# Kernel tuning notes

Hardware: AMD Instinct MI355X
Metric: run time of the kernel (lower is better)

## Reference

```python
import jax, jax.numpy as jnp
import numpy as np

B, W, H = 8, 1024, 1024
NUM_LABELS = 100  # mask ids in [0, NUM_LABELS); 0 = background
EPS = 1e-7


def setup_inputs() -> dict:
    key = jax.random.key(0)
    k1, k2 = jax.random.split(key)
    pred = jax.random.normal(k1, (B, 2, W, H), dtype=jnp.float32)
    mask = jax.random.randint(k2, (B, W, H), 0, NUM_LABELS, dtype=jnp.int32)
    ignored_map = jnp.ones((B, W, H), dtype=jnp.float32)
    return {"pred": pred, "mask": mask, "ignored_map": ignored_map}


def _smooth_l1(d):
    # SmoothL1Loss(reduction='none'), beta=1
    a = jnp.abs(d)
    return jnp.where(a < 1.0, 0.5 * d * d, a - 0.5)


def _gt_single(mask2d):
    # Vectorized replacement of the per-instance python loop:
    # segment-mean for centroids, segment-max for the per-instance `norm`.
    seg = mask2d.reshape(-1)  # [W*H]
    x_map = jnp.tile(jnp.arange(H, dtype=jnp.float32), W)    # column index (x)
    y_map = jnp.repeat(jnp.arange(W, dtype=jnp.float32), H)  # row index (y)
    cnt = jax.ops.segment_sum(jnp.ones_like(x_map), seg, num_segments=NUM_LABELS)
    safe_cnt = jnp.maximum(cnt, 1.0)
    xc = (jax.ops.segment_sum(x_map, seg, num_segments=NUM_LABELS) / safe_cnt)[seg]
    yc = (jax.ops.segment_sum(y_map, seg, num_segments=NUM_LABELS) / safe_cnt)[seg]
    fg = (seg != 0).astype(jnp.float32)  # label 0 is background (index_list[1:])
    vx = (x_map - xc) * fg  # (x_map - mean_x) * nuclei, instances are disjoint
    vy = (y_map - yc) * fg
    # torch.max over the whole image of (coord - c)*nuclei == max(seg_max, 0)
    mx = jnp.maximum(jax.ops.segment_max(vx, seg, num_segments=NUM_LABELS), 0.0)
    my = jnp.maximum(jax.ops.segment_max(vy, seg, num_segments=NUM_LABELS), 0.0)
    gx = vx / jnp.where(mx == 0.0, 1.0, mx)[seg]  # norm(): divide by max iff max != 0
    gy = vy / jnp.where(my == 0.0, 1.0, my)[seg]
    return jnp.stack([gx, gy]).reshape(2, W, H)


def reference(pred, mask, ignored_map):
    gt = jax.vmap(_gt_single)(mask)  # [B, 2, W, H]
    fg = (mask != 0).astype(jnp.float32)[:, None]  # [B, 1, W, H]
    bg = 1.0 - fg
    n = float(mask.size)
    # ((mask != 0) + 1e-07).sum() == fg_count + eps * numel
    fg_den = jnp.sum(fg) + EPS * n
    bg_den = jnp.sum(bg) + EPS * n
    d = _smooth_l1(pred - gt)
    ig = ignored_map[:, None]
    offset_loss = jnp.sum(d * ig * (fg / fg_den + bg / bg_den))
    return offset_loss, gt
```

## Files before the change

kernel.cpp:

```cpp
#include <hip/hip_runtime.h>

#define NL 100
#define BB 8
#define WW 1024
#define HH 1024
#define NPIX (WW * HH)
#define EPSF 1e-7f

#define OFF_CNT 0
#define OFF_SX  800
#define OFF_SY  1600
#define OFF_MX  2400
#define OFF_MY  3200
#define OFF_TAB 4000
#define OFF_INV 7200
#define OFF_M8  7216
#define ZERO_WORDS 4000

template<bool EMIT8>
__global__ __launch_bounds__(256) void k_stats(const int* __restrict__ mask,
                                               int* __restrict__ ws,
                                               unsigned* __restrict__ m8) {
    __shared__ unsigned s_cs[4][NL];
    __shared__ unsigned s_mx[4][NL];
    __shared__ unsigned g_cnt[NL], g_sx[NL], g_sy[NL], g_mx[NL], g_my[NL];
    const int b    = blockIdx.y;
    const int wv   = threadIdx.x >> 6;
    const int lane = threadIdx.x & 63;
    for (int i = threadIdx.x; i < NL; i += 256) {
        g_cnt[i] = 0u; g_sx[i] = 0u; g_sy[i] = 0u; g_mx[i] = 0u; g_my[i] = 0u;
    }
    for (int i = lane; i < NL; i += 64) { s_cs[wv][i] = 0u; s_mx[wv][i] = 0u; }
    __syncthreads();

    const int4* m4  = (const int4*)(mask + (size_t)b * NPIX);
    unsigned*   m8b = m8 + (size_t)b * (NPIX / 4);
    const int y0 = blockIdx.x * 8 + wv * 2;

    int4 R[2][4];
#pragma unroll
    for (int r = 0; r < 2; ++r)
#pragma unroll
        for (int it = 0; it < 4; ++it)
            R[r][it] = m4[(y0 + r) * 256 + it * 64 + lane];

#pragma unroll
    for (int r = 0; r < 2; ++r) {
        const int y = y0 + r;
#pragma unroll
        for (int it = 0; it < 4; ++it) {
            const int4 mv = R[r][it];
            const int c4 = it * 64 + lane;
            const unsigned x0 = (unsigned)(c4 << 2);
            const unsigned v0 = (1u << 21) + x0;
            atomicAdd(&s_cs[wv][mv.x], v0);     atomicMax(&s_mx[wv][mv.x], x0);
            atomicAdd(&s_cs[wv][mv.y], v0 + 1); atomicMax(&s_mx[wv][mv.y], x0 + 1);
            atomicAdd(&s_cs[wv][mv.z], v0 + 2); atomicMax(&s_mx[wv][mv.z], x0 + 2);
            atomicAdd(&s_cs[wv][mv.w], v0 + 3); atomicMax(&s_mx[wv][mv.w], x0 + 3);
            if (EMIT8)
                m8b[y * 256 + c4] = (unsigned)mv.x | ((unsigned)mv.y << 8) |
                                    ((unsigned)mv.z << 16) | ((unsigned)mv.w << 24);
        }
        for (int e = lane; e < NL; e += 64) {
            const unsigned cs  = s_cs[wv][e];
            const unsigned mx  = s_mx[wv][e];
            const unsigned cnt = cs >> 21;
            if (cnt) {
                atomicAdd(&g_cnt[e], cnt);
                atomicAdd(&g_sx[e],  cs & 0x1FFFFFu);
                atomicAdd(&g_sy[e],  cnt * (unsigned)y);
                atomicMax(&g_my[e], (unsigned)y);
            }
            if (mx) atomicMax(&g_mx[e], mx);
            s_cs[wv][e] = 0u;
            s_mx[wv][e] = 0u;
        }
    }
    __syncthreads();
    for (int e = threadIdx.x; e < NL; e += 256) {
        const unsigned cnt = g_cnt[e];
        if (cnt) {
            atomicAdd(&ws[OFF_CNT + b * NL + e], (int)cnt);
            atomicAdd(&ws[OFF_SX  + b * NL + e], (int)g_sx[e]);
            atomicAdd(&ws[OFF_SY  + b * NL + e], (int)g_sy[e]);
            atomicMax(&ws[OFF_MX  + b * NL + e], (int)g_mx[e]);
            atomicMax(&ws[OFF_MY  + b * NL + e], (int)g_my[e]);
        }
    }
}

__global__ void k_final(int* __restrict__ wsi) {
    float* wsf = (float*)wsi;
    const int t = threadIdx.x;
    if (t < BB * NL) {
        const int c = wsi[OFF_CNT + t];
        const float sc = (float)(c > 0 ? c : 1);
        const float xc = (float)wsi[OFF_SX + t] / sc;
        const float yc = (float)wsi[OFF_SY + t] / sc;
        float fmx = (float)wsi[OFF_MX + t] - xc; if (fmx < 0.0f) fmx = 0.0f;
        float fmy = (float)wsi[OFF_MY + t] - yc; if (fmy < 0.0f) fmy = 0.0f;
        float4 e;
        e.x = xc;
        e.y = yc;
        e.z = (fmx == 0.0f) ? 1.0f : 1.0f / fmx;
        e.w = (fmy == 0.0f) ? 1.0f : 1.0f / fmy;
        ((float4*)(wsf + OFF_TAB))[t] = e;
    }
    if (t == 0) {
        long long bg = 0;
        for (int b = 0; b < BB; ++b) bg += wsi[OFF_CNT + b * NL];
        const float n = (float)BB * (float)NPIX;
        const float fg_den = (float)((long long)BB * NPIX - bg) + EPSF * n;
        const float bg_den = (float)bg + EPSF * n;
        wsf[OFF_INV + 0] = 1.0f / fg_den;
        wsf[OFF_INV + 1] = 1.0f / bg_den;
    }
}

template<bool USE8>
__global__ __launch_bounds__(256) void k_loss(const int* __restrict__ mask,
                                              const unsigned* __restrict__ m8,
                                              const float* __restrict__ pred,
                                              const float* __restrict__ ig,
                                              const int* __restrict__ ws,
                                              float* __restrict__ out) {
    const float* wsf = (const float*)ws;
    __shared__ float4 s_tab[NL];
    const int b = blockIdx.y;
    for (int i = threadIdx.x; i < NL; i += 256)
        s_tab[i] = ((const float4*)(wsf + OFF_TAB))[b * NL + i];
    __syncthreads();
    const float inv_fg = wsf[OFF_INV + 0];
    const float inv_bg = wsf[OFF_INV + 1];

    const int4*     mi4 = (const int4*)(mask + (size_t)b * NPIX);
    const unsigned* m8b = m8 + (size_t)b * (NPIX / 4);
    const float4*   ig4 = (const float4*)(ig + (size_t)b * NPIX);
    const float4*   px4 = (const float4*)(pred + (size_t)(2 * b) * NPIX);
    const float4*   py4 = (const float4*)(pred + (size_t)(2 * b + 1) * NPIX);
    float* gx_out = out + 1 + (size_t)(2 * b) * NPIX;
    float* gy_out = out + 1 + (size_t)(2 * b + 1) * NPIX;

    const int base = blockIdx.x * 1024;
    unsigned M8[4]; int4 MI[4]; float4 IV[4], PX[4], PY[4];
#pragma unroll
    for (int it = 0; it < 4; ++it) {
        const int i4 = base + it * 256 + threadIdx.x;
        if (USE8) M8[it] = m8b[i4]; else MI[it] = mi4[i4];
        IV[it] = ig4[i4];
        PX[it] = px4[i4];
        PY[it] = py4[i4];
    }

    float acc = 0.0f;
#pragma unroll
    for (int it = 0; it < 4; ++it) {
        const int i4 = base + it * 256 + threadIdx.x;
        const int p  = i4 << 2;
        const float x0 = (float)(p & (HH - 1));
        const float y  = (float)(p >> 10);
        const float* igs = (const float*)&IV[it];
        const float* pxs = (const float*)&PX[it];
        const float* pys = (const float*)&PY[it];
#pragma unroll
        for (int j = 0; j < 4; ++j) {
            const int m = USE8 ? (int)((M8[it] >> (8 * j)) & 255u)
                               : ((const int*)&MI[it])[j];
            const float4 t = s_tab[m];
            const float fgf = (m != 0) ? 1.0f : 0.0f;
            const float gx = (x0 + (float)j - t.x) * t.z * fgf;
            const float gy = (y - t.y) * t.w * fgf;
            const float w  = ((m != 0) ? inv_fg : inv_bg) * igs[j];
            const float dx = pxs[j] - gx;
            const float dy = pys[j] - gy;
            const float ax = fabsf(dx), ay = fabsf(dy);
            acc += ((ax < 1.0f) ? 0.5f * dx * dx : ax - 0.5f) * w
                 + ((ay < 1.0f) ? 0.5f * dy * dy : ay - 0.5f) * w;
            __builtin_nontemporal_store(gx, &gx_out[p + j]);
            __builtin_nontemporal_store(gy, &gy_out[p + j]);
        }
    }
#pragma unroll
    for (int off = 32; off > 0; off >>= 1) acc += __shfl_down(acc, off, 64);
    __shared__ float s_part[4];
    const int lane = threadIdx.x & 63, wv = threadIdx.x >> 6;
    if (lane == 0) s_part[wv] = acc;
    __syncthreads();
    if (threadIdx.x == 0) atomicAdd(out, s_part[0] + s_part[1] + s_part[2] + s_part[3]);
}

extern "C" void kernel_launch(void* const* d_in, const int* in_sizes, int n_in,
                              void* d_out, int out_size, void* d_ws, size_t ws_size,
                              hipStream_t stream) {
    const float* pred = (const float*)d_in[0];
    const int*   mask = (const int*)d_in[1];
    const float* ig   = (const float*)d_in[2];
    float* out = (float*)d_out;
    int*   ws  = (int*)d_ws;
    unsigned* m8 = (unsigned*)(ws + OFF_M8);

    const size_t need = ((size_t)OFF_M8 + (size_t)BB * (NPIX / 4)) * 4;
    const bool use8 = ws_size >= need;

    hipMemsetAsync(d_ws, 0, ZERO_WORDS * sizeof(int), stream);
    hipMemsetAsync(d_out, 0, sizeof(float), stream);

    if (use8) k_stats<true ><<<dim3(128, BB), 256, 0, stream>>>(mask, ws, m8);
    else      k_stats<false><<<dim3(128, BB), 256, 0, stream>>>(mask, ws, m8);
    k_final<<<1, 800, 0, stream>>>(ws);
    if (use8) k_loss<true ><<<dim3(256, BB), 256, 0, stream>>>(mask, m8, pred, ig, ws, out);
    else      k_loss<false><<<dim3(256, BB), 256, 0, stream>>>(mask, m8, pred, ig, ws, out);
}
```

Measured before the change: 189.2 us.

## Replace global atomics with per-block partials reduced in parallel final kernel

k_stats now writes per-block partial statistics to a workspace array instead of doing global atomics, which removes the workspace memset and the contention on the global counters. k_final runs one block per batch and reduces the 128 partials in parallel. k_loss computes the fg/bg normalisers itself, uses nontemporal vector loads, and writes gt as 16-byte vector nontemporal stores instead of scalar ones. The max packing is merged into one shared table. The cost is extra partial-buffer traffic and a larger workspace requirement.

Result: no change. 185.6 us (-1.9%).

```diff
diff --git a/kernel.cpp b/kernel.cpp
--- a/kernel.cpp
+++ b/kernel.cpp
@@ -2,27 +2,26 @@
 
 #define NL 100
 #define BB 8
-#define WW 1024
 #define HH 1024
-#define NPIX (WW * HH)
+#define NPIX (1024 * 1024)
 #define EPSF 1e-7f
-
-#define OFF_CNT 0
-#define OFF_SX  800
-#define OFF_SY  1600
-#define OFF_MX  2400
-#define OFF_MY  3200
-#define OFF_TAB 4000
-#define OFF_INV 7200
-#define OFF_M8  7216
-#define ZERO_WORDS 4000
+#define NBLK 128
+
+typedef float f4 __attribute__((ext_vector_type(4)));
+
+#define OFF_TAB  0
+#define OFF_CNT0 3200
+#define OFF_M8   3216
+
+__device__ __forceinline__ int part_idx(int v, int blk, int b, int l) {
+    return ((v * NBLK + blk) * BB + b) * NL + l;
+}
 
 template<bool EMIT8>
 __global__ __launch_bounds__(256) void k_stats(const int* __restrict__ mask,
-                                               int* __restrict__ ws,
+                                               unsigned* __restrict__ part,
                                                unsigned* __restrict__ m8) {
-    __shared__ unsigned s_cs[4][NL];
-    __shared__ unsigned s_mx[4][NL];
+    __shared__ unsigned s_t[4][2 * NL];
     __shared__ unsigned g_cnt[NL], g_sx[NL], g_sy[NL], g_mx[NL], g_my[NL];
     const int b    = blockIdx.y;
     const int wv   = threadIdx.x >> 6;
@@ -30,7 +29,7 @@
     for (int i = threadIdx.x; i < NL; i += 256) {
         g_cnt[i] = 0u; g_sx[i] = 0u; g_sy[i] = 0u; g_mx[i] = 0u; g_my[i] = 0u;
     }
-    for (int i = lane; i < NL; i += 64) { s_cs[wv][i] = 0u; s_mx[wv][i] = 0u; }
+    for (int i = lane; i < 2 * NL; i += 64) s_t[wv][i] = 0u;
     __syncthreads();
 
     const int4* m4  = (const int4*)(mask + (size_t)b * NPIX);
@@ -44,6 +43,7 @@
         for (int it = 0; it < 4; ++it)
             R[r][it] = m4[(y0 + r) * 256 + it * 64 + lane];
 
+    unsigned* tp = &s_t[wv][0];
 #pragma unroll
     for (int r = 0; r < 2; ++r) {
         const int y = y0 + r;
@@ -51,105 +51,119 @@
         for (int it = 0; it < 4; ++it) {
             const int4 mv = R[r][it];
             const int c4 = it * 64 + lane;
-            const unsigned x0 = (unsigned)(c4 << 2);
-            const unsigned v0 = (1u << 21) + x0;
-            atomicAdd(&s_cs[wv][mv.x], v0);     atomicMax(&s_mx[wv][mv.x], x0);
-            atomicAdd(&s_cs[wv][mv.y], v0 + 1); atomicMax(&s_mx[wv][mv.y], x0 + 1);
-            atomicAdd(&s_cs[wv][mv.z], v0 + 2); atomicMax(&s_mx[wv][mv.z], x0 + 2);
-            atomicAdd(&s_cs[wv][mv.w], v0 + 3); atomicMax(&s_mx[wv][mv.w], x0 + 3);
+            const unsigned v0 = (1u << 21) + (unsigned)(c4 << 2);
+            { unsigned* p = tp + mv.x; atomicAdd(p, v0);      atomicMax(p + NL, v0); }
+            { unsigned* p = tp + mv.y; atomicAdd(p, v0 + 1u); atomicMax(p + NL, v0 + 1u); }
+            { unsigned* p = tp + mv.z; atomicAdd(p, v0 + 2u); atomicMax(p + NL, v0 + 2u); }
+            { unsigned* p = tp + mv.w; atomicAdd(p, v0 + 3u); atomicMax(p + NL, v0 + 3u); }
             if (EMIT8)
                 m8b[y * 256 + c4] = (unsigned)mv.x | ((unsigned)mv.y << 8) |
                                     ((unsigned)mv.z << 16) | ((unsigned)mv.w << 24);
         }
         for (int e = lane; e < NL; e += 64) {
-            const unsigned cs  = s_cs[wv][e];
-            const unsigned mx  = s_mx[wv][e];
-            const unsigned cnt = cs >> 21;
-            if (cnt) {
+            const unsigned cs = tp[e];
+            if (cs) {
+                const unsigned mxv = tp[e + NL];
+                const unsigned cnt = cs >> 21;
                 atomicAdd(&g_cnt[e], cnt);
                 atomicAdd(&g_sx[e],  cs & 0x1FFFFFu);
                 atomicAdd(&g_sy[e],  cnt * (unsigned)y);
-                atomicMax(&g_my[e], (unsigned)y);
+                atomicMax(&g_mx[e],  mxv & 0x1FFFFFu);
+                atomicMax(&g_my[e],  (unsigned)y);
+                tp[e] = 0u;
+                tp[e + NL] = 0u;
             }
-            if (mx) atomicMax(&g_mx[e], mx);
-            s_cs[wv][e] = 0u;
-            s_mx[wv][e] = 0u;
-        }
-    }
-    __syncthreads();
+        }
+    }
+    __syncthreads();
+    const int blk = blockIdx.x;
     for (int e = threadIdx.x; e < NL; e += 256) {
-        const unsigned cnt = g_cnt[e];
-        if (cnt) {
-            atomicAdd(&ws[OFF_CNT + b * NL + e], (int)cnt);
-            atomicAdd(&ws[OFF_SX  + b * NL + e], (int)g_sx[e]);
-            atomicAdd(&ws[OFF_SY  + b * NL + e], (int)g_sy[e]);
-            atomicMax(&ws[OFF_MX  + b * NL + e], (int)g_mx[e]);
-            atomicMax(&ws[OFF_MY  + b * NL + e], (int)g_my[e]);
-        }
-    }
-}
-
-__global__ void k_final(int* __restrict__ wsi) {
-    float* wsf = (float*)wsi;
-    const int t = threadIdx.x;
-    if (t < BB * NL) {
-        const int c = wsi[OFF_CNT + t];
-        const float sc = (float)(c > 0 ? c : 1);
-        const float xc = (float)wsi[OFF_SX + t] / sc;
-        const float yc = (float)wsi[OFF_SY + t] / sc;
-        float fmx = (float)wsi[OFF_MX + t] - xc; if (fmx < 0.0f) fmx = 0.0f;
-        float fmy = (float)wsi[OFF_MY + t] - yc; if (fmy < 0.0f) fmy = 0.0f;
-        float4 e;
+        part[part_idx(0, blk, b, e)] = g_cnt[e];
+        part[part_idx(1, blk, b, e)] = g_sx[e];
+        part[part_idx(2, blk, b, e)] = g_sy[e];
+        part[part_idx(3, blk, b, e)] = g_mx[e];
+        part[part_idx(4, blk, b, e)] = g_my[e];
+    }
+}
+
+__global__ __launch_bounds__(512) void k_final(const unsigned* __restrict__ part,
+                                               float* __restrict__ wsf) {
+    __shared__ unsigned pc[4][NL], psx[4][NL], psy[4][NL], pmx[4][NL], pmy[4][NL];
+    const int b = blockIdx.x;
+    const int q = threadIdx.x >> 7;
+    const int l = threadIdx.x & 127;
+    if (l < NL) {
+        unsigned cnt = 0, sx = 0, sy = 0, mx = 0, my = 0;
+#pragma unroll 4
+        for (int blk = q * 32; blk < q * 32 + 32; ++blk) {
+            cnt += part[part_idx(0, blk, b, l)];
+            sx  += part[part_idx(1, blk, b, l)];
+            sy  += part[part_idx(2, blk, b, l)];
+            mx = max(mx, part[part_idx(3, blk, b, l)]);
+            my = max(my, part[part_idx(4, blk, b, l)]);
+        }
+        pc[q][l] = cnt; psx[q][l] = sx; psy[q][l] = sy; pmx[q][l] = mx; pmy[q][l] = my;
+    }
+    __syncthreads();
+    if (q == 0 && l < NL) {
+        const unsigned cnt = pc[0][l] + pc[1][l] + pc[2][l] + pc[3][l];
+        const unsigned sx  = psx[0][l] + psx[1][l] + psx[2][l] + psx[3][l];
+        const unsigned sy  = psy[0][l] + psy[1][l] + psy[2][l] + psy[3][l];
+        const unsigned mx  = max(max(pmx[0][l], pmx[1][l]), max(pmx[2][l], pmx[3][l]));
+        const unsigned my  = max(max(pmy[0][l], pmy[1][l]), max(pmy[2][l], pmy[3][l]));
+        const float sc = (float)(cnt ? cnt : 1u);
+        const float xc = (float)sx / sc;
+        const float yc = (float)sy / sc;
+        float fmx = (float)mx - xc; if (fmx < 0.0f) fmx = 0.0f;
+        float fmy = (float)my - yc; if (fmy < 0.0f) fmy = 0.0f;
+        f4 e;
         e.x = xc;
         e.y = yc;
         e.z = (fmx == 0.0f) ? 1.0f : 1.0f / fmx;
         e.w = (fmy == 0.0f) ? 1.0f : 1.0f / fmy;
-        ((float4*)(wsf + OFF_TAB))[t] = e;
-    }
-    if (t == 0) {
-        long long bg = 0;
-        for (int b = 0; b < BB; ++b) bg += wsi[OFF_CNT + b * NL];
-        const float n = (float)BB * (float)NPIX;
-        const float fg_den = (float)((long long)BB * NPIX - bg) + EPSF * n;
-        const float bg_den = (float)bg + EPSF * n;
-        wsf[OFF_INV + 0] = 1.0f / fg_den;
-        wsf[OFF_INV + 1] = 1.0f / bg_den;
+        ((f4*)(wsf + OFF_TAB))[b * NL + l] = e;
+        if (l == 0) ((unsigned*)wsf)[OFF_CNT0 + b] = cnt;
     }
 }
 
 template<bool USE8>
-__global__ __launch_bounds__(256) void k_loss(const int* __restrict__ mask,
-                                              const unsigned* __restrict__ m8,
-                                              const float* __restrict__ pred,
-                                              const float* __restrict__ ig,
-                                              const int* __restrict__ ws,
-                                              float* __restrict__ out) {
-    const float* wsf = (const float*)ws;
-    __shared__ float4 s_tab[NL];
+__global__ __launch_bounds__(256, 4) void k_loss(const int* __restrict__ mask,
+                                                 const unsigned* __restrict__ m8,
+                                                 const float* __restrict__ pred,
+                                                 const float* __restrict__ ig,
+                                                 const float* __restrict__ wsf,
+                                                 float* __restrict__ out) {
+    __shared__ f4 s_tab[NL];
+    __shared__ unsigned s_c0[BB];
     const int b = blockIdx.y;
     for (int i = threadIdx.x; i < NL; i += 256)
-        s_tab[i] = ((const float4*)(wsf + OFF_TAB))[b * NL + i];
-    __syncthreads();
-    const float inv_fg = wsf[OFF_INV + 0];
-    const float inv_bg = wsf[OFF_INV + 1];
+        s_tab[i] = ((const f4*)(wsf + OFF_TAB))[b * NL + i];
+    if (threadIdx.x < BB) s_c0[threadIdx.x] = ((const unsigned*)wsf)[OFF_CNT0 + threadIdx.x];
+    __syncthreads();
+    float bgc = 0.0f;
+#pragma unroll
+    for (int i = 0; i < BB; ++i) bgc += (float)s_c0[i];
+    const float n = (float)BB * (float)NPIX;
+    const float inv_bg = 1.0f / (bgc + EPSF * n);
+    const float inv_fg = 1.0f / ((n - bgc) + EPSF * n);
 
     const int4*     mi4 = (const int4*)(mask + (size_t)b * NPIX);
     const unsigned* m8b = m8 + (size_t)b * (NPIX / 4);
-    const float4*   ig4 = (const float4*)(ig + (size_t)b * NPIX);
-    const float4*   px4 = (const float4*)(pred + (size_t)(2 * b) * NPIX);
-    const float4*   py4 = (const float4*)(pred + (size_t)(2 * b + 1) * NPIX);
-    float* gx_out = out + 1 + (size_t)(2 * b) * NPIX;
-    float* gy_out = out + 1 + (size_t)(2 * b + 1) * NPIX;
+    const f4*       ig4 = (const f4*)(ig + (size_t)b * NPIX);
+    const f4*       px4 = (const f4*)(pred + (size_t)(2 * b) * NPIX);
+    const f4*       py4 = (const f4*)(pred + (size_t)(2 * b + 1) * NPIX);
+    f4* gx4 = (f4*)(out + 1 + (size_t)(2 * b) * NPIX);
+    f4* gy4 = (f4*)(out + 1 + (size_t)(2 * b + 1) * NPIX);
 
     const int base = blockIdx.x * 1024;
-    unsigned M8[4]; int4 MI[4]; float4 IV[4], PX[4], PY[4];
+    unsigned M8[4]; int4 MI[4]; f4 IV[4], PX[4], PY[4];
 #pragma unroll
     for (int it = 0; it < 4; ++it) {
         const int i4 = base + it * 256 + threadIdx.x;
         if (USE8) M8[it] = m8b[i4]; else MI[it] = mi4[i4];
-        IV[it] = ig4[i4];
-        PX[it] = px4[i4];
-        PY[it] = py4[i4];
+        IV[it] = __builtin_nontemporal_load(&ig4[i4]);
+        PX[it] = __builtin_nontemporal_load(&px4[i4]);
+        PY[it] = __builtin_nontemporal_load(&py4[i4]);
     }
 
     float acc = 0.0f;
@@ -162,11 +176,14 @@
         const float* igs = (const float*)&IV[it];
         const float* pxs = (const float*)&PX[it];
         const float* pys = (const float*)&PY[it];
+        f4 gxv, gyv;
+        float* gxa = (float*)&gxv;
+        float* gya = (float*)&gyv;
 #pragma unroll
         for (int j = 0; j < 4; ++j) {
             const int m = USE8 ? (int)((M8[it] >> (8 * j)) & 255u)
                                : ((const int*)&MI[it])[j];
-            const float4 t = s_tab[m];
+            const f4 t = s_tab[m];
             const float fgf = (m != 0) ? 1.0f : 0.0f;
             const float gx = (x0 + (float)j - t.x) * t.z * fgf;
             const float gy = (y - t.y) * t.w * fgf;
@@ -176,9 +193,11 @@
             const float ax = fabsf(dx), ay = fabsf(dy);
             acc += ((ax < 1.0f) ? 0.5f * dx * dx : ax - 0.5f) * w
                  + ((ay < 1.0f) ? 0.5f * dy * dy : ay - 0.5f) * w;
-            __builtin_nontemporal_store(gx, &gx_out[p + j]);
-            __builtin_nontemporal_store(gy, &gy_out[p + j]);
-        }
+            gxa[j] = gx;
+            gya[j] = gy;
+        }
+        __builtin_nontemporal_store(gxv, &gx4[i4]);
+        __builtin_nontemporal_store(gyv, &gy4[i4]);
     }
 #pragma unroll
     for (int off = 32; off > 0; off >>= 1) acc += __shfl_down(acc, off, 64);
@@ -196,18 +215,19 @@
     const int*   mask = (const int*)d_in[1];
     const float* ig   = (const float*)d_in[2];
     float* out = (float*)d_out;
-    int*   ws  = (int*)d_ws;
-    unsigned* m8 = (unsigned*)(ws + OFF_M8);
-
-    const size_t need = ((size_t)OFF_M8 + (size_t)BB * (NPIX / 4)) * 4;
-    const bool use8 = ws_size >= need;
-
-    hipMemsetAsync(d_ws, 0, ZERO_WORDS * sizeof(int), stream);
-    hipMemsetAsync(d_out, 0, sizeof(float), stream);
-
-    if (use8) k_stats<true ><<<dim3(128, BB), 256, 0, stream>>>(mask, ws, m8);
-    else      k_stats<false><<<dim3(128, BB), 256, 0, stream>>>(mask, ws, m8);
-    k_final<<<1, 800, 0, stream>>>(ws);
-    if (use8) k_loss<true ><<<dim3(256, BB), 256, 0, stream>>>(mask, m8, pred, ig, ws, out);
-    else      k_loss<false><<<dim3(256, BB), 256, 0, stream>>>(mask, m8, pred, ig, ws, out);
-}
+    unsigned* wsu = (unsigned*)d_ws;
+    unsigned* m8  = wsu + OFF_M8;
+
+    const size_t part_words = 5ull * NBLK * BB * NL;
+    const size_t need8 = ((size_t)OFF_M8 + (size_t)BB * (NPIX / 4) + part_words) * 4;
+    const bool use8 = ws_size >= need8;
+    unsigned* part = use8 ? (m8 + (size_t)BB * (NPIX / 4)) : (wsu + OFF_M8);
+
+    (void)hipMemsetAsync(d_out, 0, sizeof(float), stream);
+
+    if (use8) k_stats<true ><<<dim3(NBLK, BB), 256, 0, stream>>>(mask, part, m8);
+    else      k_stats<false><<<dim3(NBLK, BB), 256, 0, stream>>>(mask, part, m8);
+    k_final<<<BB, 512, 0, stream>>>(part, (float*)d_ws);
+    if (use8) k_loss<true ><<<dim3(256, BB), 256, 0, stream>>>(mask, m8, pred, ig, (const float*)d_ws, out);
+    else      k_loss<false><<<dim3(256, BB), 256, 0, stream>>>(mask, m8, pred, ig, (const float*)d_ws, out);
+}
```
